# Kernel tuning notes

Hardware: AMD Instinct MI355X
Metric: run time of the kernel (lower is better)

The kernel has to match this reference:

```python
import jax, jax.numpy as jnp
import numpy as np

HEADS = 8
DIM_HEAD = 64
DIM = 512
EPS = 1e-5


def setup_inputs() -> dict:
    key = jax.random.key(0)
    ks = jax.random.split(key, 4)
    b, n = 4, 2048
    inner = HEADS * DIM_HEAD
    x = jax.random.normal(ks[0], (b, n, DIM), dtype=jnp.float32)
    pose_bias = jax.random.normal(ks[1], (b, n), dtype=jnp.float32)
    ln_gamma = jnp.ones((DIM,), dtype=jnp.float32)
    ln_beta = jnp.zeros((DIM,), dtype=jnp.float32)
    w_qkv = jax.random.normal(ks[2], (DIM, 3 * inner), dtype=jnp.float32) * (DIM ** -0.5)
    w_out = jax.random.normal(ks[3], (inner, DIM), dtype=jnp.float32) * (inner ** -0.5)
    beta = jnp.float32(0.5)
    return {"x": x, "pose_bias": pose_bias, "ln_gamma": ln_gamma,
            "ln_beta": ln_beta, "w_qkv": w_qkv, "w_out": w_out, "beta": beta}


def reference(x, pose_bias, ln_gamma, ln_beta, w_qkv, w_out, beta):
    b, n, d = x.shape
    h, dh = HEADS, DIM_HEAD
    scale = dh ** -0.5
    # LayerNorm (biased variance, eps=1e-5, affine)
    mu = jnp.mean(x, axis=-1, keepdims=True)
    var = jnp.mean(jnp.square(x - mu), axis=-1, keepdims=True)
    xn = (x - mu) * jax.lax.rsqrt(var + EPS) * ln_gamma + ln_beta
    # fused QKV projection (no bias)
    qkv = xn @ w_qkv                                  # [b, n, 3*h*dh]
    q, k, v = jnp.split(qkv, 3, axis=-1)
    def to_heads(t):
        return t.reshape(b, n, h, dh).transpose(0, 2, 1, 3)  # [b, h, n, dh]
    q, k, v = to_heads(q), to_heads(k), to_heads(v)
    dots = jnp.einsum('bhnd,bhmd->bhnm', q, k) * scale  # [b, h, n, n]
    # additive pose bias: beta * (bias_i + bias_j), broadcast over heads
    pose_attn = beta * (pose_bias[:, None, :, None] + pose_bias[:, None, None, :])
    dots = dots + pose_attn
    attn = jax.nn.softmax(dots, axis=-1)
    out = jnp.einsum('bhnm,bhmd->bhnd', attn, v)       # [b, h, n, dh]
    out = out.transpose(0, 2, 1, 3).reshape(b, n, h * dh)
    return out @ w_out
```

## Files before the change

### kernel.cpp

```cpp
#include <hip/hip_runtime.h>

#define NH    8
#define DH    64
#define DIMD  512
#define NCTX  2048
#define NB    4
#define NROWS (NB * NCTX)
#define QKVN  (3 * DIMD)

typedef __attribute__((ext_vector_type(8))) short bf16x8;
typedef __attribute__((ext_vector_type(4))) float f32x4;

#define INV_LN2 1.44269504f
#define SCLOG   (0.125f * INV_LN2)

__device__ __forceinline__ unsigned short f2bits(float f) {
  unsigned u = __float_as_uint(f);
  u += 0x7fffu + ((u >> 16) & 1u);
  return (unsigned short)(u >> 16);
}
__device__ __forceinline__ float bits2f(unsigned short u) {
  return __uint_as_float(((unsigned)u) << 16);
}

__global__ __launch_bounds__(256) void ln_kernel(
    const float* __restrict__ x,
    const float* __restrict__ gamma,
    const float* __restrict__ beta,
    unsigned short* __restrict__ xn) {
  const int wid  = threadIdx.x >> 6;
  const int lane = threadIdx.x & 63;
  const int row  = blockIdx.x * 4 + wid;
  const float* xr = x + (size_t)row * DIMD + lane * 8;
  float v[8];
  const float4 a = *reinterpret_cast<const float4*>(xr);
  const float4 b = *reinterpret_cast<const float4*>(xr + 4);
  v[0] = a.x; v[1] = a.y; v[2] = a.z; v[3] = a.w;
  v[4] = b.x; v[5] = b.y; v[6] = b.z; v[7] = b.w;
  float s = 0.f;
#pragma unroll
  for (int i = 0; i < 8; ++i) s += v[i];
#pragma unroll
  for (int off = 32; off; off >>= 1) s += __shfl_down(s, off);
  s = __shfl(s, 0);
  const float mu = s * (1.f / DIMD);
  float ss = 0.f;
#pragma unroll
  for (int i = 0; i < 8; ++i) { float d = v[i] - mu; ss += d * d; }
#pragma unroll
  for (int off = 32; off; off >>= 1) ss += __shfl_down(ss, off);
  ss = __shfl(ss, 0);
  const float inv = rsqrtf(ss * (1.f / DIMD) + 1e-5f);
  const float4 g0 = *reinterpret_cast<const float4*>(gamma + lane * 8);
  const float4 g1 = *reinterpret_cast<const float4*>(gamma + lane * 8 + 4);
  const float4 b0 = *reinterpret_cast<const float4*>(beta + lane * 8);
  const float4 b1 = *reinterpret_cast<const float4*>(beta + lane * 8 + 4);
  float g[8] = {g0.x, g0.y, g0.z, g0.w, g1.x, g1.y, g1.z, g1.w};
  float be[8] = {b0.x, b0.y, b0.z, b0.w, b1.x, b1.y, b1.z, b1.w};
  bf16x8 o;
#pragma unroll
  for (int i = 0; i < 8; ++i)
    o[i] = (short)f2bits((v[i] - mu) * inv * g[i] + be[i]);
  *reinterpret_cast<bf16x8*>(xn + (size_t)row * DIMD + lane * 8) = o;
}

__global__ __launch_bounds__(256) void tconv_kernel(
    const float* __restrict__ in, unsigned short* __restrict__ out, int R, int C) {
  __shared__ float T[64][65];
  const int r0 = blockIdx.y * 64, c0 = blockIdx.x * 64;
  const int ty = threadIdx.x >> 4, tx = threadIdx.x & 15;
#pragma unroll
  for (int i = 0; i < 4; ++i) {
    const int r = ty + i * 16;
    const float4 v = *reinterpret_cast<const float4*>(
        in + (size_t)(r0 + r) * C + c0 + tx * 4);
    T[r][tx * 4 + 0] = v.x; T[r][tx * 4 + 1] = v.y;
    T[r][tx * 4 + 2] = v.z; T[r][tx * 4 + 3] = v.w;
  }
  __syncthreads();
#pragma unroll
  for (int i = 0; i < 4; ++i) {
    const int c = ty + i * 16;
    ushort4 o;
    o.x = f2bits(T[tx * 4 + 0][c]); o.y = f2bits(T[tx * 4 + 1][c]);
    o.z = f2bits(T[tx * 4 + 2][c]); o.w = f2bits(T[tx * 4 + 3][c]);
    *reinterpret_cast<ushort4*>(out + (size_t)(c0 + c) * R + r0 + tx * 4) = o;
  }
}

__global__ __launch_bounds__(256) void pbprep_kernel(
    const float* __restrict__ pb, const float* __restrict__ betap,
    unsigned short* __restrict__ cexp) {
  const int i = blockIdx.x * 256 + threadIdx.x;
  cexp[i] = f2bits(exp2f(betap[0] * INV_LN2 * pb[i]));
}

__global__ __launch_bounds__(256) void vtrans_kernel(
    const unsigned short* __restrict__ qkv,
    const unsigned short* __restrict__ cexp,
    unsigned short* __restrict__ vt) {
  __shared__ unsigned short T[64][68];
  const int jt = blockIdx.x, hi = blockIdx.y, bi = blockIdx.z;
  const int ty = threadIdx.x >> 4, tx = threadIdx.x & 15;
  const int j0 = jt * 64;
#pragma unroll
  for (int i = 0; i < 4; ++i) {
    const int j = ty + i * 16;
    const ushort4 v = *reinterpret_cast<const ushort4*>(
        qkv + (size_t)(bi * NCTX + j0 + j) * QKVN + 2 * DIMD + hi * DH + tx * 4);
    T[j][tx * 4 + 0] = v.x; T[j][tx * 4 + 1] = v.y;
    T[j][tx * 4 + 2] = v.z; T[j][tx * 4 + 3] = v.w;
  }
  const ushort4 cv = *reinterpret_cast<const ushort4*>(cexp + bi * NCTX + j0 + tx * 4);
  const float c0 = bits2f(cv.x), c1 = bits2f(cv.y), c2 = bits2f(cv.z), c3 = bits2f(cv.w);
  __syncthreads();
#pragma unroll
  for (int i = 0; i < 4; ++i) {
    const int d = ty + i * 16;
    ushort4 o;
    o.x = f2bits(bits2f(T[tx * 4 + 0][d]) * c0);
    o.y = f2bits(bits2f(T[tx * 4 + 1][d]) * c1);
    o.z = f2bits(bits2f(T[tx * 4 + 2][d]) * c2);
    o.w = f2bits(bits2f(T[tx * 4 + 3][d]) * c3);
    *reinterpret_cast<ushort4*>(
        vt + ((size_t)(bi * NH + hi) * DH + d) * NCTX + j0 + tx * 4) = o;
  }
}

__device__ __forceinline__ void storeC(float* C, size_t idx, float v) { C[idx] = v; }
__device__ __forceinline__ void storeC(unsigned short* C, size_t idx, float v) { C[idx] = f2bits(v); }

template <typename CT, bool QS>
__global__ __launch_bounds__(256) void mgemm_kernel(
    const unsigned short* __restrict__ A, const unsigned short* __restrict__ Bt,
    CT* __restrict__ C, int M, int N, int K) {
  __shared__ __align__(16) unsigned short As[128][72];
  __shared__ __align__(16) unsigned short Bs[128][72];
  const int tid  = threadIdx.x;
  const int wave = tid >> 6, lane = tid & 63;
  const int quad = lane >> 4, l16 = lane & 15;
  const int wr = wave >> 1, wc = wave & 1;
  const int tm0 = blockIdx.y * 128, tn0 = blockIdx.x * 128;
  const int srow = tid >> 3;
  const int schunk = (tid & 7) * 8;
  f32x4 acc[4][4];
#pragma unroll
  for (int i = 0; i < 4; ++i)
#pragma unroll
    for (int j = 0; j < 4; ++j) acc[i][j] = (f32x4){0.f, 0.f, 0.f, 0.f};

  for (int k0 = 0; k0 < K; k0 += 64) {
#pragma unroll
    for (int p = 0; p < 4; ++p) {
      const int r = srow + p * 32;
      *reinterpret_cast<bf16x8*>(&As[r][schunk]) =
          *reinterpret_cast<const bf16x8*>(A + (size_t)(tm0 + r) * K + k0 + schunk);
      *reinterpret_cast<bf16x8*>(&Bs[r][schunk]) =
          *reinterpret_cast<const bf16x8*>(Bt + (size_t)(tn0 + r) * K + k0 + schunk);
    }
    __syncthreads();
#pragma unroll
    for (int kc = 0; kc < 2; ++kc) {
      const int kk = kc * 32 + quad * 8;
      bf16x8 af[4], bfr[4];
#pragma unroll
      for (int i = 0; i < 4; ++i)
        af[i] = *reinterpret_cast<const bf16x8*>(&As[wr * 64 + i * 16 + l16][kk]);
#pragma unroll
      for (int j = 0; j < 4; ++j)
        bfr[j] = *reinterpret_cast<const bf16x8*>(&Bs[wc * 64 + j * 16 + l16][kk]);
#pragma unroll
      for (int i = 0; i < 4; ++i)
#pragma unroll
        for (int j = 0; j < 4; ++j)
          acc[i][j] = __builtin_amdgcn_mfma_f32_16x16x32_bf16(af[i], bfr[j], acc[i][j], 0, 0, 0);
    }
    __syncthreads();
  }
#pragma unroll
  for (int j = 0; j < 4; ++j) {
    const int col = tn0 + wc * 64 + j * 16 + l16;
    const float scl = (QS && col < DIMD) ? SCLOG : 1.0f;
#pragma unroll
    for (int i = 0; i < 4; ++i)
#pragma unroll
      for (int r = 0; r < 4; ++r)
        storeC(C, (size_t)(tm0 + wr * 64 + i * 16 + quad * 4 + r) * N + col,
               acc[i][j][r] * scl);
  }
}

__global__ __launch_bounds__(256, 4) void fattn_kernel(
    const unsigned short* __restrict__ qkv,
    const unsigned short* __restrict__ vtg,
    const unsigned short* __restrict__ cexp,
    unsigned short* __restrict__ out) {
  __shared__ __align__(16) unsigned short QPs[4][16][72];
  __shared__ __align__(16) unsigned short Kl[64][72];
  __shared__ __align__(16) unsigned short Vt[80][72];
  const int qt = blockIdx.x, hi = blockIdx.y, bi = blockIdx.z;
  const int tid  = threadIdx.x;
  const int wave = tid >> 6, lane = tid & 63;
  const int quad = lane >> 4, l16 = lane & 15;
  const int qrow0 = qt * 64;
  const unsigned short* base  = qkv + (size_t)bi * NCTX * QKVN + hi * DH;
  const unsigned short* vbase = vtg + (size_t)(bi * NH + hi) * DH * NCTX;
  const unsigned short* cbase = cexp + (size_t)bi * NCTX;
  const int sr = tid >> 2;
  const int sc4 = (tid & 3) * 16;

  {
    const unsigned short* qr = base + (size_t)(qrow0 + sr) * QKVN + sc4;
    *reinterpret_cast<bf16x8*>(&QPs[sr >> 4][sr & 15][sc4]) =
        *reinterpret_cast<const bf16x8*>(qr);
    *reinterpret_cast<bf16x8*>(&QPs[sr >> 4][sr & 15][sc4 + 8]) =
        *reinterpret_cast<const bf16x8*>(qr + 8);
  }
  if (tid < 135) {
    const uint4 z = {0u, 0u, 0u, 0u};
    *reinterpret_cast<uint4*>(&Vt[65 + tid / 9][(tid % 9) * 8]) = z;
  }
  bf16x8 pk0, pk1, pv0, pv1; ushort4 pc;
  {
    const unsigned short* kr = base + (size_t)sr * QKVN + DIMD + sc4;
    pk0 = *reinterpret_cast<const bf16x8*>(kr);
    pk1 = *reinterpret_cast<const bf16x8*>(kr + 8);
    const unsigned short* vr = vbase + (size_t)sr * NCTX + sc4;
    pv0 = *reinterpret_cast<const bf16x8*>(vr);
    pv1 = *reinterpret_cast<const bf16x8*>(vr + 8);
    if (tid < 16) pc = *reinterpret_cast<const ushort4*>(cbase + tid * 4);
    *reinterpret_cast<bf16x8*>(&Kl[sr][sc4])     = pk0;
    *reinterpret_cast<bf16x8*>(&Kl[sr][sc4 + 8]) = pk1;
    *reinterpret_cast<bf16x8*>(&Vt[sr][sc4])     = pv0;
    *reinterpret_cast<bf16x8*>(&Vt[sr][sc4 + 8]) = pv1;
    if (tid < 16) *reinterpret_cast<ushort4*>(&Vt[64][tid * 4]) = pc;
  }
  __syncthreads();
  const bf16x8 qf0 = *reinterpret_cast<const bf16x8*>(&QPs[wave][l16][quad * 8]);
  const bf16x8 qf1 = *reinterpret_cast<const bf16x8*>(&QPs[wave][l16][32 + quad * 8]);

  f32x4 O[4], accl;
#pragma unroll
  for (int t = 0; t < 4; ++t) O[t] = (f32x4){0.f, 0.f, 0.f, 0.f};
  accl = (f32x4){0.f, 0.f, 0.f, 0.f};

  for (int kt = 0; kt < 32; ++kt) {
    if (kt < 31) {
      const int krow1 = (kt + 1) * 64;
      const unsigned short* kr = base + (size_t)(krow1 + sr) * QKVN + DIMD + sc4;
      pk0 = *reinterpret_cast<const bf16x8*>(kr);
      pk1 = *reinterpret_cast<const bf16x8*>(kr + 8);
      const unsigned short* vr = vbase + (size_t)sr * NCTX + krow1 + sc4;
      pv0 = *reinterpret_cast<const bf16x8*>(vr);
      pv1 = *reinterpret_cast<const bf16x8*>(vr + 8);
      if (tid < 16) pc = *reinterpret_cast<const ushort4*>(cbase + krow1 + tid * 4);
    }
    f32x4 sfr[4];
#pragma unroll
    for (int t = 0; t < 4; ++t) {
      f32x4 acc = (f32x4){0.f, 0.f, 0.f, 0.f};
      const bf16x8 kf0 = *reinterpret_cast<const bf16x8*>(&Kl[t * 16 + l16][quad * 8]);
      acc = __builtin_amdgcn_mfma_f32_16x16x32_bf16(kf0, qf0, acc, 0, 0, 0);
      const bf16x8 kf1 = *reinterpret_cast<const bf16x8*>(&Kl[t * 16 + l16][32 + quad * 8]);
      acc = __builtin_amdgcn_mfma_f32_16x16x32_bf16(kf1, qf1, acc, 0, 0, 0);
      sfr[t] = acc;
    }
#pragma unroll
    for (int t = 0; t < 4; ++t) {
      const unsigned u0 = __float_as_uint(exp2f(sfr[t][0])) + 0x8000u;
      const unsigned u1 = __float_as_uint(exp2f(sfr[t][1])) + 0x8000u;
      const unsigned u2 = __float_as_uint(exp2f(sfr[t][2])) + 0x8000u;
      const unsigned u3 = __float_as_uint(exp2f(sfr[t][3])) + 0x8000u;
      uint2 pw;
      pw.x = __builtin_amdgcn_perm(u1, u0, 0x07060302u);
      pw.y = __builtin_amdgcn_perm(u3, u2, 0x07060302u);
      *reinterpret_cast<uint2*>(&QPs[wave][l16][t * 16 + quad * 4]) = pw;
    }
#pragma unroll
    for (int jc = 0; jc < 2; ++jc) {
      const bf16x8 pf = *reinterpret_cast<const bf16x8*>(&QPs[wave][l16][jc * 32 + quad * 8]);
#pragma unroll
      for (int t = 0; t < 4; ++t) {
        const bf16x8 bv = *reinterpret_cast<const bf16x8*>(&Vt[t * 16 + l16][jc * 32 + quad * 8]);
        O[t] = __builtin_amdgcn_mfma_f32_16x16x32_bf16(pf, bv, O[t], 0, 0, 0);
      }
      const bf16x8 cf = *reinterpret_cast<const bf16x8*>(&Vt[64 + l16][jc * 32 + quad * 8]);
      accl = __builtin_amdgcn_mfma_f32_16x16x32_bf16(pf, cf, accl, 0, 0, 0);
    }
    if (kt < 31) {
      __syncthreads();
      *reinterpret_cast<bf16x8*>(&Kl[sr][sc4])     = pk0;
      *reinterpret_cast<bf16x8*>(&Kl[sr][sc4 + 8]) = pk1;
      *reinterpret_cast<bf16x8*>(&Vt[sr][sc4])     = pv0;
      *reinterpret_cast<bf16x8*>(&Vt[sr][sc4 + 8]) = pv1;
      if (tid < 16) *reinterpret_cast<ushort4*>(&Vt[64][tid * 4]) = pc;
      __syncthreads();
    }
  }
  float linv[4];
#pragma unroll
  for (int r = 0; r < 4; ++r)
    linv[r] = 1.f / __shfl(accl[r], lane & 48);
#pragma unroll
  for (int t = 0; t < 4; ++t)
#pragma unroll
    for (int r = 0; r < 4; ++r)
      out[((size_t)bi * NCTX + qrow0 + wave * 16 + quad * 4 + r) * DIMD +
          hi * DH + t * 16 + l16] = f2bits(O[t][r] * linv[r]);
}

extern "C" void kernel_launch(void* const* d_in, const int* in_sizes, int n_in,
                              void* d_out, int out_size, void* d_ws, size_t ws_size,
                              hipStream_t stream) {
  const float* x     = (const float*)d_in[0];
  const float* pose  = (const float*)d_in[1];
  const float* gam   = (const float*)d_in[2];
  const float* bet   = (const float*)d_in[3];
  const float* wqkv  = (const float*)d_in[4];
  const float* wout  = (const float*)d_in[5];
  const float* betap = (const float*)d_in[6];
  float* out = (float*)d_out;

  unsigned short* xn    = (unsigned short*)d_ws;
  unsigned short* qkvb  = xn + (size_t)NROWS * DIMD;
  unsigned short* wqkvT = qkvb + (size_t)NROWS * QKVN;
  unsigned short* woutT = wqkvT + (size_t)QKVN * DIMD;
  unsigned short* vtg   = woutT + (size_t)DIMD * DIMD;
  unsigned short* cexp  = vtg + (size_t)NB * NH * DH * NCTX;
  unsigned short* aout  = xn;

  ln_kernel<<<NROWS / 4, 256, 0, stream>>>(x, gam, bet, xn);
  tconv_kernel<<<dim3(QKVN / 64, DIMD / 64), 256, 0, stream>>>(wqkv, wqkvT, DIMD, QKVN);
  tconv_kernel<<<dim3(DIMD / 64, DIMD / 64), 256, 0, stream>>>(wout, woutT, DIMD, DIMD);
  pbprep_kernel<<<NROWS / 256, 256, 0, stream>>>(pose, betap, cexp);
  mgemm_kernel<unsigned short, true><<<dim3(QKVN / 128, NROWS / 128), 256, 0, stream>>>(
      xn, wqkvT, qkvb, NROWS, QKVN, DIMD);
  vtrans_kernel<<<dim3(NCTX / 64, NH, NB), 256, 0, stream>>>(qkvb, cexp, vtg);
  fattn_kernel<<<dim3(NCTX / 64, NH, NB), 256, 0, stream>>>(qkvb, vtg, cexp, aout);
  mgemm_kernel<float, false><<<dim3(DIMD / 128, NROWS / 128), 256, 0, stream>>>(
      aout, woutT, out, NROWS, DIMD, DIMD);
}
```

Baseline: 196.3 us.

## Split attention waves over query and key halves; prefetch GEMM tiles into registers

```diff
diff --git a/kernel.cpp b/kernel.cpp
--- a/kernel.cpp
+++ b/kernel.cpp
@@ -149,16 +149,29 @@
 #pragma unroll
     for (int j = 0; j < 4; ++j) acc[i][j] = (f32x4){0.f, 0.f, 0.f, 0.f};
 
+  bf16x8 ra[4], rb[4];
+#pragma unroll
+  for (int p = 0; p < 4; ++p) {
+    const int r = srow + p * 32;
+    ra[p] = *reinterpret_cast<const bf16x8*>(A + (size_t)(tm0 + r) * K + schunk);
+    rb[p] = *reinterpret_cast<const bf16x8*>(Bt + (size_t)(tn0 + r) * K + schunk);
+  }
   for (int k0 = 0; k0 < K; k0 += 64) {
 #pragma unroll
     for (int p = 0; p < 4; ++p) {
       const int r = srow + p * 32;
-      *reinterpret_cast<bf16x8*>(&As[r][schunk]) =
-          *reinterpret_cast<const bf16x8*>(A + (size_t)(tm0 + r) * K + k0 + schunk);
-      *reinterpret_cast<bf16x8*>(&Bs[r][schunk]) =
-          *reinterpret_cast<const bf16x8*>(Bt + (size_t)(tn0 + r) * K + k0 + schunk);
+      *reinterpret_cast<bf16x8*>(&As[r][schunk]) = ra[p];
+      *reinterpret_cast<bf16x8*>(&Bs[r][schunk]) = rb[p];
     }
     __syncthreads();
+    if (k0 + 64 < K) {
+#pragma unroll
+      for (int p = 0; p < 4; ++p) {
+        const int r = srow + p * 32;
+        ra[p] = *reinterpret_cast<const bf16x8*>(A + (size_t)(tm0 + r) * K + k0 + 64 + schunk);
+        rb[p] = *reinterpret_cast<const bf16x8*>(Bt + (size_t)(tn0 + r) * K + k0 + 64 + schunk);
+      }
+    }
 #pragma unroll
     for (int kc = 0; kc < 2; ++kc) {
       const int kk = kc * 32 + quad * 8;
@@ -195,13 +208,18 @@
     const unsigned short* __restrict__ vtg,
     const unsigned short* __restrict__ cexp,
     unsigned short* __restrict__ out) {
-  __shared__ __align__(16) unsigned short QPs[4][16][72];
-  __shared__ __align__(16) unsigned short Kl[64][72];
-  __shared__ __align__(16) unsigned short Vt[80][72];
+  __shared__ __align__(16) unsigned short lds[19840];
+  unsigned short (*Kl)[72] = (unsigned short (*)[72])(lds + 5120);
+  unsigned short (*Vt)[72] = (unsigned short (*)[72])(lds + 9728);
+  unsigned short* Ob = lds + 15488;
+  float* lb = (float*)(lds + 19584);
+
   const int qt = blockIdx.x, hi = blockIdx.y, bi = blockIdx.z;
   const int tid  = threadIdx.x;
   const int wave = tid >> 6, lane = tid & 63;
   const int quad = lane >> 4, l16 = lane & 15;
+  const int wq = wave & 1, wk = wave >> 1;
+  unsigned short* Pw = lds + wave * 1280;
   const int qrow0 = qt * 64;
   const unsigned short* base  = qkv + (size_t)bi * NCTX * QKVN + hi * DH;
   const unsigned short* vbase = vtg + (size_t)(bi * NH + hi) * DH * NCTX;
@@ -209,13 +227,13 @@
   const int sr = tid >> 2;
   const int sc4 = (tid & 3) * 16;
 
-  {
-    const unsigned short* qr = base + (size_t)(qrow0 + sr) * QKVN + sc4;
-    *reinterpret_cast<bf16x8*>(&QPs[sr >> 4][sr & 15][sc4]) =
-        *reinterpret_cast<const bf16x8*>(qr);
-    *reinterpret_cast<bf16x8*>(&QPs[sr >> 4][sr & 15][sc4 + 8]) =
-        *reinterpret_cast<const bf16x8*>(qr + 8);
-  }
+  bf16x8 qf[2][2];
+#pragma unroll
+  for (int u = 0; u < 2; ++u)
+#pragma unroll
+    for (int h = 0; h < 2; ++h)
+      qf[u][h] = *reinterpret_cast<const bf16x8*>(
+          base + (size_t)(qrow0 + wq * 32 + u * 16 + l16) * QKVN + h * 32 + quad * 8);
   if (tid < 135) {
     const uint4 z = {0u, 0u, 0u, 0u};
     *reinterpret_cast<uint4*>(&Vt[65 + tid / 9][(tid % 9) * 8]) = z;
@@ -236,13 +254,14 @@
     if (tid < 16) *reinterpret_cast<ushort4*>(&Vt[64][tid * 4]) = pc;
   }
   __syncthreads();
-  const bf16x8 qf0 = *reinterpret_cast<const bf16x8*>(&QPs[wave][l16][quad * 8]);
-  const bf16x8 qf1 = *reinterpret_cast<const bf16x8*>(&QPs[wave][l16][32 + quad * 8]);
-
-  f32x4 O[4], accl;
-#pragma unroll
-  for (int t = 0; t < 4; ++t) O[t] = (f32x4){0.f, 0.f, 0.f, 0.f};
-  accl = (f32x4){0.f, 0.f, 0.f, 0.f};
+
+  f32x4 O[2][4], accl[2];
+#pragma unroll
+  for (int u = 0; u < 2; ++u) {
+    accl[u] = (f32x4){0.f, 0.f, 0.f, 0.f};
+#pragma unroll
+    for (int s = 0; s < 4; ++s) O[u][s] = (f32x4){0.f, 0.f, 0.f, 0.f};
+  }
 
   for (int kt = 0; kt < 32; ++kt) {
     if (kt < 31) {
@@ -255,37 +274,49 @@
       pv1 = *reinterpret_cast<const bf16x8*>(vr + 8);
       if (tid < 16) pc = *reinterpret_cast<const ushort4*>(cbase + krow1 + tid * 4);
     }
-    f32x4 sfr[4];
-#pragma unroll
-    for (int t = 0; t < 4; ++t) {
-      f32x4 acc = (f32x4){0.f, 0.f, 0.f, 0.f};
-      const bf16x8 kf0 = *reinterpret_cast<const bf16x8*>(&Kl[t * 16 + l16][quad * 8]);
-      acc = __builtin_amdgcn_mfma_f32_16x16x32_bf16(kf0, qf0, acc, 0, 0, 0);
-      const bf16x8 kf1 = *reinterpret_cast<const bf16x8*>(&Kl[t * 16 + l16][32 + quad * 8]);
-      acc = __builtin_amdgcn_mfma_f32_16x16x32_bf16(kf1, qf1, acc, 0, 0, 0);
-      sfr[t] = acc;
-    }
-#pragma unroll
-    for (int t = 0; t < 4; ++t) {
-      const unsigned u0 = __float_as_uint(exp2f(sfr[t][0])) + 0x8000u;
-      const unsigned u1 = __float_as_uint(exp2f(sfr[t][1])) + 0x8000u;
-      const unsigned u2 = __float_as_uint(exp2f(sfr[t][2])) + 0x8000u;
-      const unsigned u3 = __float_as_uint(exp2f(sfr[t][3])) + 0x8000u;
-      uint2 pw;
-      pw.x = __builtin_amdgcn_perm(u1, u0, 0x07060302u);
-      pw.y = __builtin_amdgcn_perm(u3, u2, 0x07060302u);
-      *reinterpret_cast<uint2*>(&QPs[wave][l16][t * 16 + quad * 4]) = pw;
-    }
-#pragma unroll
-    for (int jc = 0; jc < 2; ++jc) {
-      const bf16x8 pf = *reinterpret_cast<const bf16x8*>(&QPs[wave][l16][jc * 32 + quad * 8]);
-#pragma unroll
-      for (int t = 0; t < 4; ++t) {
-        const bf16x8 bv = *reinterpret_cast<const bf16x8*>(&Vt[t * 16 + l16][jc * 32 + quad * 8]);
-        O[t] = __builtin_amdgcn_mfma_f32_16x16x32_bf16(pf, bv, O[t], 0, 0, 0);
+    f32x4 sfr[2][2];
+#pragma unroll
+    for (int t = 0; t < 2; ++t) {
+      const bf16x8 kf0 = *reinterpret_cast<const bf16x8*>(
+          &Kl[wk * 32 + t * 16 + l16][quad * 8]);
+      const bf16x8 kf1 = *reinterpret_cast<const bf16x8*>(
+          &Kl[wk * 32 + t * 16 + l16][32 + quad * 8]);
+#pragma unroll
+      for (int u = 0; u < 2; ++u) {
+        f32x4 acc = (f32x4){0.f, 0.f, 0.f, 0.f};
+        acc = __builtin_amdgcn_mfma_f32_16x16x32_bf16(kf0, qf[u][0], acc, 0, 0, 0);
+        acc = __builtin_amdgcn_mfma_f32_16x16x32_bf16(kf1, qf[u][1], acc, 0, 0, 0);
+        sfr[t][u] = acc;
       }
-      const bf16x8 cf = *reinterpret_cast<const bf16x8*>(&Vt[64 + l16][jc * 32 + quad * 8]);
-      accl = __builtin_amdgcn_mfma_f32_16x16x32_bf16(pf, cf, accl, 0, 0, 0);
+    }
+#pragma unroll
+    for (int t = 0; t < 2; ++t)
+#pragma unroll
+      for (int u = 0; u < 2; ++u) {
+        const unsigned u0 = __float_as_uint(exp2f(sfr[t][u][0])) + 0x8000u;
+        const unsigned u1 = __float_as_uint(exp2f(sfr[t][u][1])) + 0x8000u;
+        const unsigned u2 = __float_as_uint(exp2f(sfr[t][u][2])) + 0x8000u;
+        const unsigned u3 = __float_as_uint(exp2f(sfr[t][u][3])) + 0x8000u;
+        uint2 pw;
+        pw.x = __builtin_amdgcn_perm(u1, u0, 0x07060302u);
+        pw.y = __builtin_amdgcn_perm(u3, u2, 0x07060302u);
+        *reinterpret_cast<uint2*>(&Pw[(u * 16 + l16) * 40 + t * 16 + quad * 4]) = pw;
+      }
+    {
+      const bf16x8 cf = *reinterpret_cast<const bf16x8*>(
+          &Vt[64 + l16][wk * 32 + quad * 8]);
+#pragma unroll
+      for (int u = 0; u < 2; ++u) {
+        const bf16x8 pf = *reinterpret_cast<const bf16x8*>(
+            &Pw[(u * 16 + l16) * 40 + quad * 8]);
+#pragma unroll
+        for (int s = 0; s < 4; ++s) {
+          const bf16x8 bv = *reinterpret_cast<const bf16x8*>(
+              &Vt[s * 16 + l16][wk * 32 + quad * 8]);
+          O[u][s] = __builtin_amdgcn_mfma_f32_16x16x32_bf16(pf, bv, O[u][s], 0, 0, 0);
+        }
+        accl[u] = __builtin_amdgcn_mfma_f32_16x16x32_bf16(pf, cf, accl[u], 0, 0, 0);
+      }
     }
     if (kt < 31) {
       __syncthreads();
@@ -297,16 +328,43 @@
       __syncthreads();
     }
   }
-  float linv[4];
-#pragma unroll
-  for (int r = 0; r < 4; ++r)
-    linv[r] = 1.f / __shfl(accl[r], lane & 48);
-#pragma unroll
-  for (int t = 0; t < 4; ++t)
-#pragma unroll
-    for (int r = 0; r < 4; ++r)
-      out[((size_t)bi * NCTX + qrow0 + wave * 16 + quad * 4 + r) * DIMD +
-          hi * DH + t * 16 + l16] = f2bits(O[t][r] * linv[r]);
+  __syncthreads();
+  if (wk == 1) {
+#pragma unroll
+    for (int u = 0; u < 2; ++u) {
+#pragma unroll
+      for (int s = 0; s < 4; ++s)
+#pragma unroll
+        for (int r = 0; r < 4; ++r)
+          Ob[(wq * 32 + u * 16 + quad * 4 + r) * 64 + s * 16 + l16] = f2bits(O[u][s][r]);
+      if (l16 == 0)
+#pragma unroll
+        for (int r = 0; r < 4; ++r)
+          lb[64 + wq * 32 + u * 16 + quad * 4 + r] = accl[u][r];
+    }
+  } else {
+#pragma unroll
+    for (int u = 0; u < 2; ++u)
+      if (l16 == 0)
+#pragma unroll
+        for (int r = 0; r < 4; ++r)
+          lb[wq * 32 + u * 16 + quad * 4 + r] = accl[u][r];
+  }
+  __syncthreads();
+  if (wk == 0) {
+#pragma unroll
+    for (int u = 0; u < 2; ++u)
+#pragma unroll
+      for (int r = 0; r < 4; ++r) {
+        const int ql = wq * 32 + u * 16 + quad * 4 + r;
+        const float linv = 1.f / (lb[ql] + lb[64 + ql]);
+        const size_t orow = ((size_t)bi * NCTX + qrow0 + ql) * DIMD + hi * DH;
+#pragma unroll
+        for (int s = 0; s < 4; ++s)
+          out[orow + s * 16 + l16] =
+              f2bits((O[u][s][r] + bits2f(Ob[ql * 64 + s * 16 + l16])) * linv);
+      }
+  }
 }
 
 extern "C" void kernel_launch(void* const* d_in, const int* in_sizes, int n_in,
```

Measured after the change: 181.8 us. 1.08x faster.
